# Optimization experiments

Measured on AMD Instinct MI355X. Metric: run time of the kernel, lower is better.

Reference implementation:

```python
import math
import jax, jax.numpy as jnp
import numpy as np

MAX_LEN = 2048
D_HEAD = 64
B, H, S = 4, 16, 1024


def setup_inputs() -> dict:
    key = jax.random.key(0)
    kq, kk, kp = jax.random.split(key, 3)
    q = jax.random.normal(kq, (B, H, S, D_HEAD), dtype=jnp.float32)
    k = jax.random.normal(kk, (B, H, S, D_HEAD), dtype=jnp.float32)
    pos_table = jax.random.normal(kp, (MAX_LEN, D_HEAD), dtype=jnp.float32)
    return {"q": q, "k": k, "pos_table": pos_table}


def reference(q, k, pos_table):
    d_head = q.shape[-1]
    seq_len = q.shape[2]
    max_len = pos_table.shape[0]
    scale = 1.0 / math.sqrt(d_head)
    # attention gates: (b,h,s,s)
    gates = jax.nn.sigmoid(jnp.einsum('bhsd,bhtd->bhst', q, k) * scale)
    # context positions: weighted sum of key indices -> (b,h,s)
    positions = jnp.arange(seq_len, dtype=q.dtype)
    ctx_pos = jnp.einsum('bhst,t->bhs', gates, positions)
    ctx_pos = jnp.clip(ctx_pos, 0.0, float(max_len - 2))
    pos_floor = ctx_pos.astype(jnp.int32)  # (b,h,s)
    pos_frac = (ctx_pos - pos_floor.astype(q.dtype))[..., None]  # (b,h,s,1)
    emb_floor = pos_table[pos_floor]  # (b,h,s,d)
    emb_ceil = pos_table[jnp.minimum(pos_floor + 1, max_len - 1)]
    pos_emb = emb_floor + pos_frac * (emb_ceil - emb_floor)  # (b,h,s,d)
    # bias: (b,h,s,s)
    bias = jnp.einsum('bhsd,bhtd->bhst', q, pos_emb)
    return bias
```

## Files before the change

### kernel.cpp

```cpp
#include <hip/hip_runtime.h>

#define Bb_ 4
#define Hh_ 16
#define Ss_ 1024
#define DH 64
#define MAXLEN 2048
#define BH (Bb_*Hh_)
#define LDST 72
#define SW 132

typedef __attribute__((ext_vector_type(8))) short short8;
typedef __attribute__((ext_vector_type(4))) float floatx4;
typedef __attribute__((ext_vector_type(4))) unsigned short ushort4v;

static __device__ __forceinline__ unsigned short f2bf(float f) {
    unsigned int u = __builtin_bit_cast(unsigned int, f);
    u = (u + 0x7fffu + ((u >> 16) & 1u)) >> 16;
    return (unsigned short)u;
}

static __device__ __forceinline__ void stage_tile(unsigned short* lds,
                                                  const float* __restrict__ g,
                                                  int tid) {
#pragma unroll
    for (int it = 0; it < 8; ++it) {
        int idx = it * 1024 + tid * 4;
        int row = idx >> 6, col = idx & 63;
        const float4 v = *reinterpret_cast<const float4*>(g + row * 64 + col);
        ushort4v o = { f2bf(v.x), f2bf(v.y), f2bf(v.z), f2bf(v.w) };
        *reinterpret_cast<ushort4v*>(lds + row * LDST + col) = o;
    }
}

__global__ __launch_bounds__(256, 2)
void ctx_kernel(const float* __restrict__ q, const float* __restrict__ k,
                float* __restrict__ ctx, float2* __restrict__ mm) {
    __shared__ __align__(16) unsigned short Ab[128 * LDST];
    __shared__ __align__(16) unsigned short Kb[2][128 * LDST];
    __shared__ float sh_ctx[128];

    int bx = blockIdx.x;
    int bh = bx & 63, mt = bx >> 6;
    int m0 = mt << 7;
    int tid = threadIdx.x;
    int lane = tid & 63, w = tid >> 6;
    int lo = lane & 15, quad = lane >> 4;

    const float* kb = k + (size_t)bh * Ss_ * DH;

    stage_tile(Ab, q + (size_t)(bh * Ss_ + m0) * DH, tid);
    stage_tile(Kb[0], kb, tid);
    __syncthreads();

    short8 afr[2][2];
#pragma unroll
    for (int i = 0; i < 2; ++i)
#pragma unroll
        for (int k2 = 0; k2 < 2; ++k2)
            afr[i][k2] = *reinterpret_cast<const short8*>(
                &Ab[(w * 32 + i * 16 + lo) * LDST + k2 * 32 + quad * 8]);

    float rp[2][4];
#pragma unroll
    for (int i = 0; i < 2; ++i)
#pragma unroll
        for (int r = 0; r < 4; ++r) rp[i][r] = 0.f;

    const float kSig = -0.18033688011112042f;

#pragma unroll 1
    for (int tt = 0; tt < 8; ++tt) {
        const unsigned short* cur = Kb[tt & 1];
        if (tt < 7) stage_tile(Kb[(tt + 1) & 1], kb + (size_t)(tt + 1) * 128 * DH, tid);

        int t0 = tt << 7;
#pragma unroll
        for (int j = 0; j < 8; ++j) {
            short8 b0 = *reinterpret_cast<const short8*>(
                &cur[(j * 16 + lo) * LDST + 0 + quad * 8]);
            short8 b1 = *reinterpret_cast<const short8*>(
                &cur[(j * 16 + lo) * LDST + 32 + quad * 8]);
            float tcol = (float)(t0 + j * 16 + lo);
#pragma unroll
            for (int i = 0; i < 2; ++i) {
                floatx4 c = {0.f, 0.f, 0.f, 0.f};
                c = __builtin_amdgcn_mfma_f32_16x16x32_bf16(afr[i][0], b0, c, 0, 0, 0);
                c = __builtin_amdgcn_mfma_f32_16x16x32_bf16(afr[i][1], b1, c, 0, 0, 0);
#pragma unroll
                for (int r = 0; r < 4; ++r) {
                    float e = __builtin_amdgcn_exp2f(c[r] * kSig);
                    float g = __builtin_amdgcn_rcpf(1.0f + e);
                    rp[i][r] = fmaf(g, tcol, rp[i][r]);
                }
            }
        }
        __syncthreads();
    }

#pragma unroll
    for (int i = 0; i < 2; ++i)
#pragma unroll
        for (int r = 0; r < 4; ++r) {
            float v = rp[i][r];
            v += __shfl_xor(v, 1);
            v += __shfl_xor(v, 2);
            v += __shfl_xor(v, 4);
            v += __shfl_xor(v, 8);
            rp[i][r] = v;
        }

    if (lo == 0) {
#pragma unroll
        for (int i = 0; i < 2; ++i)
#pragma unroll
            for (int r = 0; r < 4; ++r) {
                int lr = w * 32 + i * 16 + quad * 4 + r;
                float v = fminf(fmaxf(rp[i][r], 0.f), (float)(MAXLEN - 2));
                sh_ctx[lr] = v;
                ctx[bh * Ss_ + m0 + lr] = v;
            }
    }
    __syncthreads();

    if (tid < 64) {
        float a = sh_ctx[tid], b = sh_ctx[tid + 64];
        float mn = fminf(a, b), mx = fmaxf(a, b);
#pragma unroll
        for (int off = 1; off < 64; off <<= 1) {
            mn = fminf(mn, __shfl_xor(mn, off));
            mx = fmaxf(mx, __shfl_xor(mx, off));
        }
        if (tid == 0) mm[bh * 8 + mt] = make_float2(mn, mx);
    }
}

__global__ __launch_bounds__(256, 4)
void bias_kernel(const float* __restrict__ q, const float* __restrict__ tb,
                 const float* __restrict__ ctx, const float2* __restrict__ mm,
                 float* __restrict__ out) {
    __shared__ __align__(16) unsigned char smem[2 * 128 * LDST * 2];

    int bx = blockIdx.x;
    int bh = bx >> 6;
    int mt = (bx >> 3) & 7;
    int nt = bx & 7;
    int m0 = mt << 7, n0 = nt << 7;
    int tid = threadIdx.x;
    int lane = tid & 63, w = tid >> 6;
    int lo = lane & 15, quad = lane >> 4;

    float mn = 3.0e38f, mx = -3.0e38f;
#pragma unroll
    for (int j = 0; j < 8; ++j) {
        float2 p = mm[bh * 8 + j];
        mn = fminf(mn, p.x);
        mx = fmaxf(mx, p.y);
    }

    if (mn == mx) {
        float* pr = reinterpret_cast<float*>(smem);
        float* sc = pr + 64;

        float v = mn;
        int fl = (int)v;
        float fr = v - (float)fl;
        int ce = min(fl + 1, MAXLEN - 1);
        if (tid < 16) {
            int d0 = tid * 4;
            const float4 e0 = *reinterpret_cast<const float4*>(tb + fl * DH + d0);
            const float4 e1 = *reinterpret_cast<const float4*>(tb + ce * DH + d0);
            pr[d0 + 0] = e0.x + fr * (e1.x - e0.x);
            pr[d0 + 1] = e0.y + fr * (e1.y - e0.y);
            pr[d0 + 2] = e0.z + fr * (e1.z - e0.z);
            pr[d0 + 3] = e0.w + fr * (e1.w - e0.w);
        }
        __syncthreads();

        {
            int row = tid >> 1, half = tid & 1;
            const float* qr = q + (size_t)(bh * Ss_ + m0 + row) * DH + half * 32;
            const float* ph = pr + half * 32;
            float s = 0.f;
#pragma unroll
            for (int d = 0; d < 32; d += 4) {
                const float4 qq = *reinterpret_cast<const float4*>(qr + d);
                s += qq.x * ph[d] + qq.y * ph[d + 1] + qq.z * ph[d + 2] +
                     qq.w * ph[d + 3];
            }
            s += __shfl_xor(s, 1);
            if (half == 0) sc[row] = s;
        }
        __syncthreads();

#pragma unroll
        for (int it = 0; it < 16; ++it) {
            int flat = (it * 256 + tid) * 4;
            int lrow = flat >> 7, col = flat & 127;
            float c = sc[lrow];
            floatx4 vv = {c, c, c, c};
            __builtin_nontemporal_store(
                vv, reinterpret_cast<floatx4*>(
                        out + (size_t)(bh * Ss_ + m0 + lrow) * Ss_ + n0 + col));
        }
        return;
    }

    unsigned short* Ab = reinterpret_cast<unsigned short*>(smem);
    unsigned short* Pb = Ab + 128 * LDST;
    float* scratch = reinterpret_cast<float*>(smem);

    stage_tile(Ab, q + (size_t)(bh * Ss_ + m0) * DH, tid);

    {
        int rsub = tid >> 4;
        int d0 = (tid & 15) * 4;
#pragma unroll
        for (int pass = 0; pass < 8; ++pass) {
            int row = pass * 16 + rsub;
            float c = ctx[bh * Ss_ + n0 + row];
            int fl = (int)c;
            float fr = c - (float)fl;
            int ce = min(fl + 1, MAXLEN - 1);
            const float4 e0 = *reinterpret_cast<const float4*>(tb + fl * DH + d0);
            const float4 e1 = *reinterpret_cast<const float4*>(tb + ce * DH + d0);
            ushort4v o = { f2bf(e0.x + fr * (e1.x - e0.x)),
                           f2bf(e0.y + fr * (e1.y - e0.y)),
                           f2bf(e0.z + fr * (e1.z - e0.z)),
                           f2bf(e0.w + fr * (e1.w - e0.w)) };
            *reinterpret_cast<ushort4v*>(&Pb[row * LDST + d0]) = o;
        }
    }
    __syncthreads();

    short8 afr[2][2];
#pragma unroll
    for (int i = 0; i < 2; ++i)
#pragma unroll
        for (int k2 = 0; k2 < 2; ++k2)
            afr[i][k2] = *reinterpret_cast<const short8*>(
                &Ab[(w * 32 + i * 16 + lo) * LDST + k2 * 32 + quad * 8]);

    floatx4 acc[2][8];
#pragma unroll
    for (int i = 0; i < 2; ++i)
#pragma unroll
        for (int j = 0; j < 8; ++j) acc[i][j] = (floatx4){0.f, 0.f, 0.f, 0.f};

#pragma unroll
    for (int j = 0; j < 8; ++j) {
        short8 b0 = *reinterpret_cast<const short8*>(
            &Pb[(j * 16 + lo) * LDST + 0 + quad * 8]);
        short8 b1 = *reinterpret_cast<const short8*>(
            &Pb[(j * 16 + lo) * LDST + 32 + quad * 8]);
#pragma unroll
        for (int i = 0; i < 2; ++i) {
            acc[i][j] = __builtin_amdgcn_mfma_f32_16x16x32_bf16(afr[i][0], b0, acc[i][j], 0, 0, 0);
            acc[i][j] = __builtin_amdgcn_mfma_f32_16x16x32_bf16(afr[i][1], b1, acc[i][j], 0, 0, 0);
        }
    }

#pragma unroll
    for (int i = 0; i < 2; ++i) {
        __syncthreads();
#pragma unroll
        for (int j = 0; j < 8; ++j)
#pragma unroll
            for (int r = 0; r < 4; ++r) {
                int lrow = w * 16 + quad * 4 + r;
                scratch[lrow * SW + j * 16 + lo] = acc[i][j][r];
            }
        __syncthreads();
#pragma unroll
        for (int it = 0; it < 8; ++it) {
            int flat = it * 1024 + tid * 4;
            int lrow = flat >> 7, col = flat & 127;
            floatx4 vv = *reinterpret_cast<const floatx4*>(&scratch[lrow * SW + col]);
            int grow = m0 + (lrow >> 4) * 32 + i * 16 + (lrow & 15);
            __builtin_nontemporal_store(
                vv, reinterpret_cast<floatx4*>(
                        out + (size_t)(bh * Ss_ + grow) * Ss_ + n0 + col));
        }
    }
}

extern "C" void kernel_launch(void* const* d_in, const int* in_sizes, int n_in,
                              void* d_out, int out_size, void* d_ws, size_t ws_size,
                              hipStream_t stream) {
    const float* q  = (const float*)d_in[0];
    const float* k  = (const float*)d_in[1];
    const float* tb = (const float*)d_in[2];
    float* ctx = (float*)d_ws;
    float2* mm = (float2*)((float*)d_ws + BH * Ss_);
    float* out = (float*)d_out;

    ctx_kernel<<<BH * 8, 256, 0, stream>>>(q, k, ctx, mm);
    bias_kernel<<<BH * 64, 256, 0, stream>>>(q, tb, ctx, mm, out);
}
```

Before: 322.1 us.

## Fuse context-position and bias kernels into a single per-column-tile kernel

Merges the two kernels into one. Each block computes clipped context positions for its 128-row tile, then loops over all 8 query tiles to write that column tile of the bias. The global ctx/min-max workspace and the second launch go away, and the uniform-value shortcut is now decided per tile from shared memory. In exchange, the output-writing phase runs on 512 blocks instead of 4096, each looping sequentially with barriers, which may reduce memory-level parallelism for the large output store.

```diff
diff --git a/kernel.cpp b/kernel.cpp
--- a/kernel.cpp
+++ b/kernel.cpp
@@ -33,23 +33,32 @@
 }
 
 __global__ __launch_bounds__(256, 2)
-void ctx_kernel(const float* __restrict__ q, const float* __restrict__ k,
-                float* __restrict__ ctx, float2* __restrict__ mm) {
-    __shared__ __align__(16) unsigned short Ab[128 * LDST];
-    __shared__ __align__(16) unsigned short Kb[2][128 * LDST];
+void cope_kernel(const float* __restrict__ q, const float* __restrict__ k,
+                 const float* __restrict__ tb, float* __restrict__ out) {
+    __shared__ __align__(16) unsigned char smem[73728];
     __shared__ float sh_ctx[128];
+    __shared__ float sh_sc[128];
+    __shared__ float2 sh_mm;
+
+    unsigned short* Ab = reinterpret_cast<unsigned short*>(smem);
+    unsigned short* Kb0 = reinterpret_cast<unsigned short*>(smem + 18432);
+    unsigned short* Kb1 = reinterpret_cast<unsigned short*>(smem + 36864);
+    float* scratch = reinterpret_cast<float*>(smem + 18432);
+    unsigned short* Pb = reinterpret_cast<unsigned short*>(smem + 55296);
+    float* pr = sh_sc;
 
     int bx = blockIdx.x;
-    int bh = bx & 63, mt = bx >> 6;
-    int m0 = mt << 7;
+    int bh = bx & 63, nt = bx >> 6;
+    int n0 = nt << 7;
     int tid = threadIdx.x;
     int lane = tid & 63, w = tid >> 6;
     int lo = lane & 15, quad = lane >> 4;
 
     const float* kb = k + (size_t)bh * Ss_ * DH;
-
-    stage_tile(Ab, q + (size_t)(bh * Ss_ + m0) * DH, tid);
-    stage_tile(Kb[0], kb, tid);
+    const float* qb = q + (size_t)bh * Ss_ * DH;
+
+    stage_tile(Ab, qb + (size_t)n0 * DH, tid);
+    stage_tile(Kb0, kb, tid);
     __syncthreads();
 
     short8 afr[2][2];
@@ -70,8 +79,9 @@
 
 #pragma unroll 1
     for (int tt = 0; tt < 8; ++tt) {
-        const unsigned short* cur = Kb[tt & 1];
-        if (tt < 7) stage_tile(Kb[(tt + 1) & 1], kb + (size_t)(tt + 1) * 128 * DH, tid);
+        const unsigned short* cur = (tt & 1) ? Kb1 : Kb0;
+        if (tt < 7)
+            stage_tile((tt & 1) ? Kb0 : Kb1, kb + (size_t)(tt + 1) * 128 * DH, tid);
 
         int t0 = tt << 7;
 #pragma unroll
@@ -115,9 +125,7 @@
 #pragma unroll
             for (int r = 0; r < 4; ++r) {
                 int lr = w * 32 + i * 16 + quad * 4 + r;
-                float v = fminf(fmaxf(rp[i][r], 0.f), (float)(MAXLEN - 2));
-                sh_ctx[lr] = v;
-                ctx[bh * Ss_ + m0 + lr] = v;
+                sh_ctx[lr] = fminf(fmaxf(rp[i][r], 0.f), (float)(MAXLEN - 2));
             }
     }
     __syncthreads();
@@ -130,38 +138,14 @@
             mn = fminf(mn, __shfl_xor(mn, off));
             mx = fmaxf(mx, __shfl_xor(mx, off));
         }
-        if (tid == 0) mm[bh * 8 + mt] = make_float2(mn, mx);
-    }
-}
-
-__global__ __launch_bounds__(256, 4)
-void bias_kernel(const float* __restrict__ q, const float* __restrict__ tb,
-                 const float* __restrict__ ctx, const float2* __restrict__ mm,
-                 float* __restrict__ out) {
-    __shared__ __align__(16) unsigned char smem[2 * 128 * LDST * 2];
-
-    int bx = blockIdx.x;
-    int bh = bx >> 6;
-    int mt = (bx >> 3) & 7;
-    int nt = bx & 7;
-    int m0 = mt << 7, n0 = nt << 7;
-    int tid = threadIdx.x;
-    int lane = tid & 63, w = tid >> 6;
-    int lo = lane & 15, quad = lane >> 4;
-
-    float mn = 3.0e38f, mx = -3.0e38f;
-#pragma unroll
-    for (int j = 0; j < 8; ++j) {
-        float2 p = mm[bh * 8 + j];
-        mn = fminf(mn, p.x);
-        mx = fmaxf(mx, p.y);
-    }
-
-    if (mn == mx) {
-        float* pr = reinterpret_cast<float*>(smem);
-        float* sc = pr + 64;
-
-        float v = mn;
+        if (tid == 0) sh_mm = make_float2(mn, mx);
+    }
+    __syncthreads();
+
+    float2 mmv = sh_mm;
+
+    if (mmv.x == mmv.y) {
+        float v = mmv.x;
         int fl = (int)v;
         float fr = v - (float)fl;
         int ce = min(fl + 1, MAXLEN - 1);
@@ -176,40 +160,46 @@
         }
         __syncthreads();
 
+        float ph[32];
         {
-            int row = tid >> 1, half = tid & 1;
-            const float* qr = q + (size_t)(bh * Ss_ + m0 + row) * DH + half * 32;
-            const float* ph = pr + half * 32;
-            float s = 0.f;
-#pragma unroll
-            for (int d = 0; d < 32; d += 4) {
-                const float4 qq = *reinterpret_cast<const float4*>(qr + d);
-                s += qq.x * ph[d] + qq.y * ph[d + 1] + qq.z * ph[d + 2] +
-                     qq.w * ph[d + 3];
-            }
-            s += __shfl_xor(s, 1);
-            if (half == 0) sc[row] = s;
-        }
-        __syncthreads();
-
-#pragma unroll
-        for (int it = 0; it < 16; ++it) {
-            int flat = (it * 256 + tid) * 4;
-            int lrow = flat >> 7, col = flat & 127;
-            float c = sc[lrow];
-            floatx4 vv = {c, c, c, c};
-            __builtin_nontemporal_store(
-                vv, reinterpret_cast<floatx4*>(
-                        out + (size_t)(bh * Ss_ + m0 + lrow) * Ss_ + n0 + col));
+            int half = tid & 1;
+#pragma unroll
+            for (int d = 0; d < 32; ++d) ph[d] = pr[half * 32 + d];
+        }
+
+#pragma unroll 1
+        for (int mt = 0; mt < 8; ++mt) {
+            int m0 = mt << 7;
+            {
+                int row = tid >> 1, half = tid & 1;
+                const float* qr = qb + (size_t)(m0 + row) * DH + half * 32;
+                float s = 0.f;
+#pragma unroll
+                for (int d = 0; d < 32; d += 4) {
+                    const float4 qq = *reinterpret_cast<const float4*>(qr + d);
+                    s += qq.x * ph[d] + qq.y * ph[d + 1] + qq.z * ph[d + 2] +
+                         qq.w * ph[d + 3];
+                }
+                s += __shfl_xor(s, 1);
+                if (half == 0) sh_sc[64 + (row >> 1)] = 0.f;
+                if (half == 0) sh_ctx[row] = s;
+            }
+            __syncthreads();
+
+#pragma unroll
+            for (int it = 0; it < 16; ++it) {
+                int flat = (it * 256 + tid) * 4;
+                int lrow = flat >> 7, col = flat & 127;
+                float c = sh_ctx[lrow];
+                floatx4 vv = {c, c, c, c};
+                __builtin_nontemporal_store(
+                    vv, reinterpret_cast<floatx4*>(
+                            out + (size_t)(bh * Ss_ + m0 + lrow) * Ss_ + n0 + col));
+            }
+            __syncthreads();
         }
         return;
     }
-
-    unsigned short* Ab = reinterpret_cast<unsigned short*>(smem);
-    unsigned short* Pb = Ab + 128 * LDST;
-    float* scratch = reinterpret_cast<float*>(smem);
-
-    stage_tile(Ab, q + (size_t)(bh * Ss_ + m0) * DH, tid);
 
     {
         int rsub = tid >> 4;
@@ -217,7 +207,7 @@
 #pragma unroll
         for (int pass = 0; pass < 8; ++pass) {
             int row = pass * 16 + rsub;
-            float c = ctx[bh * Ss_ + n0 + row];
+            float c = sh_ctx[row];
             int fl = (int)c;
             float fr = c - (float)fl;
             int ce = min(fl + 1, MAXLEN - 1);
@@ -232,54 +222,69 @@
     }
     __syncthreads();
 
-    short8 afr[2][2];
-#pragma unroll
-    for (int i = 0; i < 2; ++i)
-#pragma unroll
-        for (int k2 = 0; k2 < 2; ++k2)
-            afr[i][k2] = *reinterpret_cast<const short8*>(
-                &Ab[(w * 32 + i * 16 + lo) * LDST + k2 * 32 + quad * 8]);
-
-    floatx4 acc[2][8];
-#pragma unroll
-    for (int i = 0; i < 2; ++i)
-#pragma unroll
-        for (int j = 0; j < 8; ++j) acc[i][j] = (floatx4){0.f, 0.f, 0.f, 0.f};
-
+    short8 bfr[8][2];
 #pragma unroll
     for (int j = 0; j < 8; ++j) {
-        short8 b0 = *reinterpret_cast<const short8*>(
+        bfr[j][0] = *reinterpret_cast<const short8*>(
             &Pb[(j * 16 + lo) * LDST + 0 + quad * 8]);
-        short8 b1 = *reinterpret_cast<const short8*>(
+        bfr[j][1] = *reinterpret_cast<const short8*>(
             &Pb[(j * 16 + lo) * LDST + 32 + quad * 8]);
+    }
+
+#pragma unroll 1
+    for (int mt = 0; mt < 8; ++mt) {
+        int m0 = mt << 7;
+        stage_tile(Ab, qb + (size_t)m0 * DH, tid);
+        __syncthreads();
+
+        short8 mfr[2][2];
+#pragma unroll
+        for (int i = 0; i < 2; ++i)
+#pragma unroll
+            for (int k2 = 0; k2 < 2; ++k2)
+                mfr[i][k2] = *reinterpret_cast<const short8*>(
+                    &Ab[(w * 32 + i * 16 + lo) * LDST + k2 * 32 + quad * 8]);
+
+        floatx4 acc[2][8];
+#pragma unroll
+        for (int i = 0; i < 2; ++i)
+#pragma unroll
+            for (int j = 0; j < 8; ++j) acc[i][j] = (floatx4){0.f, 0.f, 0.f, 0.f};
+
+#pragma unroll
+        for (int j = 0; j < 8; ++j)
+#pragma unroll
+            for (int i = 0; i < 2; ++i) {
+                acc[i][j] = __builtin_amdgcn_mfma_f32_16x16x32_bf16(
+                    mfr[i][0], bfr[j][0], acc[i][j], 0, 0, 0);
+                acc[i][j] = __builtin_amdgcn_mfma_f32_16x16x32_bf16(
+                    mfr[i][1], bfr[j][1], acc[i][j], 0, 0, 0);
+            }
+
 #pragma unroll
         for (int i = 0; i < 2; ++i) {
-            acc[i][j] = __builtin_amdgcn_mfma_f32_16x16x32_bf16(afr[i][0], b0, acc[i][j], 0, 0, 0);
-            acc[i][j] = __builtin_amdgcn_mfma_f32_16x16x32_bf16(afr[i][1], b1, acc[i][j], 0, 0, 0);
-        }
-    }
-
-#pragma unroll
-    for (int i = 0; i < 2; ++i) {
+            __syncthreads();
+#pragma unroll
+            for (int j = 0; j < 8; ++j)
+#pragma unroll
+                for (int r = 0; r < 4; ++r) {
+                    int lrow = w * 16 + quad * 4 + r;
+                    scratch[lrow * SW + j * 16 + lo] = acc[i][j][r];
+                }
+            __syncthreads();
+#pragma unroll
+            for (int it = 0; it < 8; ++it) {
+                int flat = it * 1024 + tid * 4;
+                int lrow = flat >> 7, col = flat & 127;
+                floatx4 vv =
+                    *reinterpret_cast<const floatx4*>(&scratch[lrow * SW + col]);
+                int grow = m0 + (lrow >> 4) * 32 + i * 16 + (lrow & 15);
+                __builtin_nontemporal_store(
+                    vv, reinterpret_cast<floatx4*>(
+                            out + (size_t)(bh * Ss_ + grow) * Ss_ + n0 + col));
+            }
+        }
         __syncthreads();
-#pragma unroll
-        for (int j = 0; j < 8; ++j)
-#pragma unroll
-            for (int r = 0; r < 4; ++r) {
-                int lrow = w * 16 + quad * 4 + r;
-                scratch[lrow * SW + j * 16 + lo] = acc[i][j][r];
-            }
-        __syncthreads();
-#pragma unroll
-        for (int it = 0; it < 8; ++it) {
-            int flat = it * 1024 + tid * 4;
-            int lrow = flat >> 7, col = flat & 127;
-            floatx4 vv = *reinterpret_cast<const floatx4*>(&scratch[lrow * SW + col]);
-            int grow = m0 + (lrow >> 4) * 32 + i * 16 + (lrow & 15);
-            __builtin_nontemporal_store(
-                vv, reinterpret_cast<floatx4*>(
-                        out + (size_t)(bh * Ss_ + grow) * Ss_ + n0 + col));
-        }
     }
 }
 
@@ -289,10 +294,7 @@
     const float* q  = (const float*)d_in[0];
     const float* k  = (const float*)d_in[1];
     const float* tb = (const float*)d_in[2];
-    float* ctx = (float*)d_ws;
-    float2* mm = (float2*)((float*)d_ws + BH * Ss_);
     float* out = (float*)d_out;
 
-    ctx_kernel<<<BH * 8, 256, 0, stream>>>(q, k, ctx, mm);
-    bias_kernel<<<BH * 64, 256, 0, stream>>>(q, tb, ctx, mm, out);
+    cope_kernel<<<BH * 8, 256, 0, stream>>>(q, k, tb, out);
 }
```

Measured after the change: 310.5 us. 3.6% less time.
